# Performance work log

Measured on AMD Instinct MI355X. Metric: run time of the kernel, lower is better.

Reference implementation:

```python
import jax, jax.numpy as jnp
import numpy as np

CHANNELS = [4096, 4096, 4096, 4096]
SPARSITY = 0.9  # fraction of weight entries zeroed (sten.random_mask_sparsify frac)
BATCH = 4096


def _sparse_weight(key, out_f, in_f, frac):
    kw, km = jax.random.split(key)
    w = jax.random.normal(kw, (out_f, in_f), dtype=jnp.float32)
    keep = jax.random.uniform(km, (out_f, in_f)) >= frac  # keep ~(1-frac) entries
    return jnp.where(keep, w, 0.0)


def setup_inputs() -> dict:
    key = jax.random.key(0)
    ks = jax.random.split(key, 7)
    x = jax.random.normal(ks[0], (BATCH, CHANNELS[0]), dtype=jnp.float32)
    W1 = _sparse_weight(ks[1], CHANNELS[1], CHANNELS[0], SPARSITY)
    b1 = jax.random.uniform(ks[2], (CHANNELS[1],), dtype=jnp.float32)
    W2 = _sparse_weight(ks[3], CHANNELS[2], CHANNELS[1], SPARSITY)
    b2 = jax.random.uniform(ks[4], (CHANNELS[2],), dtype=jnp.float32)
    W3 = _sparse_weight(ks[5], CHANNELS[3], CHANNELS[2], SPARSITY)
    b3 = jax.random.uniform(ks[6], (CHANNELS[3],), dtype=jnp.float32)
    return {"x": x, "W1": W1, "b1": b1, "W2": W2, "b2": b2, "W3": W3, "b3": b3}


def reference(x, W1, b1, W2, b2, W3, b3):
    # Sequential: Linear -> ReLU -> Linear -> ReLU -> Linear
    # F.linear(x, W, b) == x @ W.T + b; weights already carry the sparsity mask.
    h = x @ W1.T + b1
    h = jax.nn.relu(h)
    h = h @ W2.T + b2
    h = jax.nn.relu(h)
    return h @ W3.T + b3
```

## Files before the change

kernel.cpp:

```cpp
#include <hip/hip_runtime.h>
#include <cstdint>


#define MATN 4096
#define NT (MATN / 64)

typedef _Float16 half8 __attribute__((ext_vector_type(8)));
typedef float f32x4 __attribute__((ext_vector_type(4)));

__device__ __forceinline__ void glds16(const void* g, void* l) {
    __builtin_amdgcn_global_load_lds(
        (const __attribute__((address_space(1))) char*)(uintptr_t)g,
        (__attribute__((address_space(3))) char*)(uintptr_t)l,
        16, 0, 0);
}

__device__ __forceinline__ void cvtblk_body(const float* __restrict__ in,
                                            _Float16* __restrict__ out, int n16) {
    for (int g = blockIdx.x * 256 + threadIdx.x; g < n16; g += gridDim.x * 256) {
        const int r16 = g & 15;
        const int kq  = (g >> 4) & 3;
        const int ks  = (g >> 6) & 1;
        const int T   = (g >> 7) & 63;
        const int R   = g >> 13;
        const size_t row = (size_t)R * 16 + r16;
        const int    col = T * 64 + ks * 32 + kq * 8;
        const float* p = in + row * MATN + col;
        float4 a = *(const float4*)p;
        float4 b = *(const float4*)(p + 4);
        half8 o;
        o[0] = (_Float16)a.x; o[1] = (_Float16)a.y;
        o[2] = (_Float16)a.z; o[3] = (_Float16)a.w;
        o[4] = (_Float16)b.x; o[5] = (_Float16)b.y;
        o[6] = (_Float16)b.z; o[7] = (_Float16)b.w;
        *(half8*)(out + (size_t)g * 8) = o;
    }
}

__global__ __launch_bounds__(256)
void cvt_blk(const float* __restrict__ in, _Float16* __restrict__ out, int n16) {
    cvtblk_body(in, out, n16);
}

__global__ __launch_bounds__(256)
void cvt_blk2(const float* __restrict__ i0, _Float16* __restrict__ o0,
              const float* __restrict__ i1, _Float16* __restrict__ o1, int n16) {
    cvtblk_body(blockIdx.y ? i1 : i0, blockIdx.y ? o1 : o0, n16);
}

__global__ __launch_bounds__(256)
void cvt_blk4(const float* __restrict__ i0, _Float16* __restrict__ o0,
              const float* __restrict__ i1, _Float16* __restrict__ o1,
              const float* __restrict__ i2, _Float16* __restrict__ o2,
              const float* __restrict__ i3, _Float16* __restrict__ o3, int n16) {
    const float* in;
    _Float16* out;
    switch (blockIdx.y) {
        case 0: in = i0; out = o0; break;
        case 1: in = i1; out = o1; break;
        case 2: in = i2; out = o2; break;
        default: in = i3; out = o3; break;
    }
    cvtblk_body(in, out, n16);
}

#define MFMA_(d, x, y) d = __builtin_amdgcn_mfma_f32_16x16x32_f16(x, y, d, 0, 0, 0)

template <bool RELU, bool OBLK, typename OutT>
__global__ __launch_bounds__(512, 2)
void gemm_blk(const _Float16* __restrict__ A, const _Float16* __restrict__ B,
              const float* __restrict__ bias, OutT* __restrict__ C) {
    __shared__ _Float16 lds[2][4][128 * 64];

    const int tid  = threadIdx.x;
    const int lane = tid & 63;
    const int w    = tid >> 6;
    const int wm   = w >> 2;
    const int wn   = w & 3;
    const int l16  = lane & 15;
    const int kq   = lane >> 4;

    const int bid   = blockIdx.y * 16 + blockIdx.x;
    const int sbid  = (bid & 7) * 32 + (bid >> 3);
    const int tileM = (sbid >> 4) * 256;
    const int tileN = (sbid & 15) * 256;

    char* const ldsb = (char*)lds;

    const int lb = lane * 16;
    const char* const aSrc =
        (const char*)A + ((size_t)((tileM >> 4) + w) * 131072) + lb;
    const char* const bSrc =
        (const char*)B + ((size_t)((tileN >> 4) + w) * 131072) + lb;
    const int wj = w * 2048;

#define SA(Tt, h, j)                                                           \
    do {                                                                       \
        if ((Tt) < NT)                                                         \
            glds16(aSrc + (size_t)(h)*1048576 + (size_t)(Tt)*2048 + (j)*1024,  \
                   ldsb + ((Tt)&1) * 65536 + (h)*49152 + wj + (j)*1024);       \
    } while (0)
#define SB(Tt, h, j)                                                           \
    do {                                                                       \
        if ((Tt) < NT)                                                         \
            glds16(bSrc + (size_t)(h)*1048576 + (size_t)(Tt)*2048 + (j)*1024,  \
                   ldsb + ((Tt)&1) * 65536 + 16384 + (h)*16384 + wj +          \
                       (j)*1024);                                              \
    } while (0)

    half8 aP[4], bP[4], bQ[4];
    f32x4 acc[8][4] = {};

    SA(0, 0, 0); SA(0, 1, 0);
    SB(0, 0, 0); SB(0, 1, 0);
    SA(0, 0, 1); SA(0, 1, 1);
    SB(0, 0, 1); SB(0, 1, 1);
    asm volatile("s_waitcnt vmcnt(4)" ::: "memory");
    __builtin_amdgcn_s_barrier();

    for (int T = 0; T < NT; ++T) {
        const char* bufb = ldsb + (T & 1) * 65536;
        const char* Ard  = bufb + wm * 49152 + lb;
        const char* Brd  = bufb + 16384 + (wn >> 1) * 16384 + (wn & 1) * 8192 + lb;

#pragma unroll
        for (int i = 0; i < 4; ++i) aP[i] = *(const half8*)(Ard + i * 2048);
#pragma unroll
        for (int n = 0; n < 4; ++n) bP[n] = *(const half8*)(Brd + n * 2048);
        SA(T + 1, 0, 0); SA(T + 1, 1, 0);
        __builtin_amdgcn_s_barrier();
        asm volatile("s_waitcnt lgkmcnt(0)" ::: "memory");
        __builtin_amdgcn_sched_barrier(0);
        __builtin_amdgcn_s_setprio(1);
#pragma unroll
        for (int i = 0; i < 4; ++i)
#pragma unroll
            for (int n = 0; n < 4; ++n) MFMA_(acc[i][n], aP[i], bP[n]);
        __builtin_amdgcn_s_setprio(0);
        __builtin_amdgcn_s_barrier();

#pragma unroll
        for (int i = 0; i < 4; ++i)
            aP[i] = *(const half8*)(Ard + 8192 + i * 2048);
        SB(T + 1, 0, 0); SB(T + 1, 1, 0);
        __builtin_amdgcn_s_barrier();
        asm volatile("s_waitcnt lgkmcnt(0)" ::: "memory");
        __builtin_amdgcn_sched_barrier(0);
        __builtin_amdgcn_s_setprio(1);
#pragma unroll
        for (int i = 0; i < 4; ++i)
#pragma unroll
            for (int n = 0; n < 4; ++n) MFMA_(acc[4 + i][n], aP[i], bP[n]);
        __builtin_amdgcn_s_setprio(0);
        if (T < NT - 1)
            asm volatile("s_waitcnt vmcnt(4)" ::: "memory");
        else
            asm volatile("s_waitcnt vmcnt(0)" ::: "memory");
        __builtin_amdgcn_s_barrier();

#pragma unroll
        for (int i = 0; i < 4; ++i)
            aP[i] = *(const half8*)(Ard + 9216 + i * 2048);
#pragma unroll
        for (int n = 0; n < 4; ++n)
            bQ[n] = *(const half8*)(Brd + 1024 + n * 2048);
        SA(T + 1, 0, 1); SA(T + 1, 1, 1);
        __builtin_amdgcn_s_barrier();
        asm volatile("s_waitcnt lgkmcnt(0)" ::: "memory");
        __builtin_amdgcn_sched_barrier(0);
        __builtin_amdgcn_s_setprio(1);
#pragma unroll
        for (int i = 0; i < 4; ++i)
#pragma unroll
            for (int n = 0; n < 4; ++n) MFMA_(acc[4 + i][n], aP[i], bQ[n]);
        __builtin_amdgcn_s_setprio(0);
        __builtin_amdgcn_s_barrier();

#pragma unroll
        for (int i = 0; i < 4; ++i)
            aP[i] = *(const half8*)(Ard + 1024 + i * 2048);
        SB(T + 1, 0, 1); SB(T + 1, 1, 1);
        __builtin_amdgcn_s_barrier();
        asm volatile("s_waitcnt lgkmcnt(0)" ::: "memory");
        __builtin_amdgcn_sched_barrier(0);
        __builtin_amdgcn_s_setprio(1);
#pragma unroll
        for (int i = 0; i < 4; ++i)
#pragma unroll
            for (int n = 0; n < 4; ++n) MFMA_(acc[i][n], aP[i], bQ[n]);
        __builtin_amdgcn_s_setprio(0);
        asm volatile("s_waitcnt vmcnt(4)" ::: "memory");
        __builtin_amdgcn_s_barrier();
    }
#undef SA
#undef SB

    if (OBLK) {
        char* const Cb = (char*)C;
        const int tN0 = tileN >> 6;
#pragma unroll
        for (int ni = 0; ni < 4; ++ni) {
            const int q  = ni * 16 + l16;
            const float bv = bias[tileN + wn * 64 + q];
            const size_t colOff = (size_t)(((tN0 + wn) * 2 + ((q >> 5) & 1))) * 1024 +
                                  ((q >> 3) & 3) * 256 + (q & 7) * 2;
#pragma unroll
            for (int mi = 0; mi < 8; ++mi) {
                const size_t Roff =
                    (size_t)((tileM >> 4) + wm * 8 + mi) * 131072;
#pragma unroll
                for (int r = 0; r < 4; ++r) {
                    float v = acc[mi][ni][r] + bv;
                    if (RELU) v = v > 0.f ? v : 0.f;
                    *(_Float16*)(Cb + Roff + colOff + (kq * 4 + r) * 16) =
                        (_Float16)v;
                }
            }
        }
    } else {
#pragma unroll
        for (int ni = 0; ni < 4; ++ni) {
            const int gn = tileN + wn * 64 + ni * 16 + l16;
            const float bv = bias[gn];
#pragma unroll
            for (int mi = 0; mi < 8; ++mi) {
                const int gm = tileM + wm * 128 + mi * 16 + kq * 4;
#pragma unroll
                for (int r = 0; r < 4; ++r) {
                    float v = acc[mi][ni][r] + bv;
                    if (RELU) v = v > 0.f ? v : 0.f;
                    C[(size_t)(gm + r) * MATN + gn] = (OutT)v;
                }
            }
        }
    }
}

extern "C" void kernel_launch(void* const* d_in, const int* in_sizes, int n_in,
                              void* d_out, int out_size, void* d_ws, size_t ws_size,
                              hipStream_t stream) {
    const float* x  = (const float*)d_in[0];
    const float* W1 = (const float*)d_in[1];
    const float* b1 = (const float*)d_in[2];
    const float* W2 = (const float*)d_in[3];
    const float* b2 = (const float*)d_in[4];
    const float* W3 = (const float*)d_in[5];
    const float* b3 = (const float*)d_in[6];
    float* out = (float*)d_out;

    const size_t MAT = (size_t)MATN * MATN;
    const size_t HB  = MAT * 2;
    const int n16 = (int)(MAT / 8);
    dim3 ggrid(MATN / 256, MATN / 256);

    if (ws_size >= HB * 5) {
        _Float16* xb = (_Float16*)d_ws;
        _Float16* w1 = (_Float16*)((char*)d_ws + HB);
        _Float16* w2 = (_Float16*)((char*)d_ws + HB * 2);
        _Float16* w3 = (_Float16*)((char*)d_ws + HB * 3);
        _Float16* h1 = (_Float16*)((char*)d_ws + HB * 4);
        _Float16* h2 = xb;

        cvt_blk4<<<dim3(8192, 4), 256, 0, stream>>>(x, xb, W1, w1, W2, w2,
                                                    W3, w3, n16);
        gemm_blk<true, true, _Float16><<<ggrid, 512, 0, stream>>>(xb, w1, b1, h1);
        gemm_blk<true, true, _Float16><<<ggrid, 512, 0, stream>>>(h1, w2, b2, h2);
        gemm_blk<false, false, float><<<ggrid, 512, 0, stream>>>(h2, w3, b3, out);
    } else {
        _Float16* xb = (_Float16*)d_ws;
        _Float16* wb = (_Float16*)((char*)d_ws + HB);
        _Float16* h1 = (_Float16*)((char*)d_ws + HB * 2);
        _Float16* h2 = xb;

        cvt_blk2<<<dim3(8192, 2), 256, 0, stream>>>(x, xb, W1, wb, n16);
        gemm_blk<true, true, _Float16><<<ggrid, 512, 0, stream>>>(xb, wb, b1, h1);
        cvt_blk<<<8192, 256, 0, stream>>>(W2, wb, n16);
        gemm_blk<true, true, _Float16><<<ggrid, 512, 0, stream>>>(h1, wb, b2, h2);
        cvt_blk<<<8192, 256, 0, stream>>>(W3, wb, n16);
        gemm_blk<false, false, float><<<ggrid, 512, 0, stream>>>(h2, wb, b3, out);
    }
}
```

Baseline: 577.9 us.

## Load A fragments directly into registers, stage only B in LDS

The GEMM now loads each wave's A operand straight from global memory into registers, since every wave owns distinct rows, and stages only the B tile in LDS. This halves LDS capacity and traffic and removes most per-phase barriers. The wave layout changes from 2x4 to 4x2, with each wave covering 64x128. The conversion kernel is reorganised so each wave handles one 512-element block unit, and the grid is shrunk to match. Trade-offs: more VGPR pressure from the extra prefetch registers, and A global-load latency now sits directly on the MFMA dependency chain.

```diff
diff --git a/kernel.cpp b/kernel.cpp
--- a/kernel.cpp
+++ b/kernel.cpp
@@ -16,16 +16,16 @@
 }
 
 __device__ __forceinline__ void cvtblk_body(const float* __restrict__ in,
-                                            _Float16* __restrict__ out, int n16) {
-    for (int g = blockIdx.x * 256 + threadIdx.x; g < n16; g += gridDim.x * 256) {
-        const int r16 = g & 15;
-        const int kq  = (g >> 4) & 3;
-        const int ks  = (g >> 6) & 1;
-        const int T   = (g >> 7) & 63;
-        const int R   = g >> 13;
-        const size_t row = (size_t)R * 16 + r16;
-        const int    col = T * 64 + ks * 32 + kq * 8;
-        const float* p = in + row * MATN + col;
+                                            _Float16* __restrict__ out,
+                                            int nunits) {
+    const int lane = threadIdx.x & 63;
+    const int r16 = lane & 15, kq = lane >> 4;
+    const int wv = (blockIdx.x * 256 + (int)threadIdx.x) >> 6;
+    const int nw = (gridDim.x * 256) >> 6;
+    for (int u = wv; u < nunits; u += nw) {
+        const int ks = u & 1, T = (u >> 1) & 63, R = u >> 7;
+        const float* p =
+            in + (size_t)(R * 16 + r16) * MATN + T * 64 + ks * 32 + kq * 8;
         float4 a = *(const float4*)p;
         float4 b = *(const float4*)(p + 4);
         half8 o;
@@ -33,26 +33,26 @@
         o[2] = (_Float16)a.z; o[3] = (_Float16)a.w;
         o[4] = (_Float16)b.x; o[5] = (_Float16)b.y;
         o[6] = (_Float16)b.z; o[7] = (_Float16)b.w;
-        *(half8*)(out + (size_t)g * 8) = o;
+        *(half8*)(out + (size_t)u * 512 + lane * 8) = o;
     }
 }
 
 __global__ __launch_bounds__(256)
-void cvt_blk(const float* __restrict__ in, _Float16* __restrict__ out, int n16) {
-    cvtblk_body(in, out, n16);
+void cvt_blk(const float* __restrict__ in, _Float16* __restrict__ out, int nu) {
+    cvtblk_body(in, out, nu);
 }
 
 __global__ __launch_bounds__(256)
 void cvt_blk2(const float* __restrict__ i0, _Float16* __restrict__ o0,
-              const float* __restrict__ i1, _Float16* __restrict__ o1, int n16) {
-    cvtblk_body(blockIdx.y ? i1 : i0, blockIdx.y ? o1 : o0, n16);
+              const float* __restrict__ i1, _Float16* __restrict__ o1, int nu) {
+    cvtblk_body(blockIdx.y ? i1 : i0, blockIdx.y ? o1 : o0, nu);
 }
 
 __global__ __launch_bounds__(256)
 void cvt_blk4(const float* __restrict__ i0, _Float16* __restrict__ o0,
               const float* __restrict__ i1, _Float16* __restrict__ o1,
               const float* __restrict__ i2, _Float16* __restrict__ o2,
-              const float* __restrict__ i3, _Float16* __restrict__ o3, int n16) {
+              const float* __restrict__ i3, _Float16* __restrict__ o3, int nu) {
     const float* in;
     _Float16* out;
     switch (blockIdx.y) {
@@ -61,22 +61,22 @@
         case 2: in = i2; out = o2; break;
         default: in = i3; out = o3; break;
     }
-    cvtblk_body(in, out, n16);
+    cvtblk_body(in, out, nu);
 }
 
 #define MFMA_(d, x, y) d = __builtin_amdgcn_mfma_f32_16x16x32_f16(x, y, d, 0, 0, 0)
 
 template <bool RELU, bool OBLK, typename OutT>
 __global__ __launch_bounds__(512, 2)
-void gemm_blk(const _Float16* __restrict__ A, const _Float16* __restrict__ B,
-              const float* __restrict__ bias, OutT* __restrict__ C) {
-    __shared__ _Float16 lds[2][4][128 * 64];
+void gemm_areg(const _Float16* __restrict__ A, const _Float16* __restrict__ B,
+               const float* __restrict__ bias, OutT* __restrict__ C) {
+    __shared__ _Float16 ldsB[2][16384];
 
     const int tid  = threadIdx.x;
     const int lane = tid & 63;
     const int w    = tid >> 6;
-    const int wm   = w >> 2;
-    const int wn   = w & 3;
+    const int wm   = w >> 1;
+    const int wn   = w & 1;
     const int l16  = lane & 15;
     const int kq   = lane >> 4;
 
@@ -85,132 +85,125 @@
     const int tileM = (sbid >> 4) * 256;
     const int tileN = (sbid & 15) * 256;
 
-    char* const ldsb = (char*)lds;
-
+    char* const ldsb = (char*)ldsB;
     const int lb = lane * 16;
-    const char* const aSrc =
-        (const char*)A + ((size_t)((tileM >> 4) + w) * 131072) + lb;
+
     const char* const bSrc =
-        (const char*)B + ((size_t)((tileN >> 4) + w) * 131072) + lb;
-    const int wj = w * 2048;
-
-#define SA(Tt, h, j)                                                           \
+        (const char*)B + (size_t)((tileN >> 4) + w) * 131072 + lb;
+#define SB(Tt, g, j)                                                           \
     do {                                                                       \
         if ((Tt) < NT)                                                         \
-            glds16(aSrc + (size_t)(h)*1048576 + (size_t)(Tt)*2048 + (j)*1024,  \
-                   ldsb + ((Tt)&1) * 65536 + (h)*49152 + wj + (j)*1024);       \
+            glds16(bSrc + (size_t)(g)*1048576 + (size_t)(Tt)*2048 + (j)*1024,  \
+                   ldsb + ((Tt)&1) * 32768 + ((g)*8 + w) * 2048 + (j)*1024);   \
     } while (0)
-#define SB(Tt, h, j)                                                           \
+
+    const char* const aSrc =
+        (const char*)A + (size_t)((tileM >> 4) + wm * 4) * 131072 + lb;
+#define LA(dst, Tt, ks_)                                                       \
     do {                                                                       \
-        if ((Tt) < NT)                                                         \
-            glds16(bSrc + (size_t)(h)*1048576 + (size_t)(Tt)*2048 + (j)*1024,  \
-                   ldsb + ((Tt)&1) * 65536 + 16384 + (h)*16384 + wj +          \
-                       (j)*1024);                                              \
+        if ((Tt) < NT) {                                                       \
+            _Pragma("unroll") for (int i_ = 0; i_ < 4; ++i_) dst[i_] =         \
+                *(const half8*)(aSrc + (size_t)i_ * 131072 +                   \
+                                (size_t)(Tt)*2048 + (ks_)*1024);               \
+        }                                                                      \
     } while (0)
 
-    half8 aP[4], bP[4], bQ[4];
-    f32x4 acc[8][4] = {};
-
-    SA(0, 0, 0); SA(0, 1, 0);
-    SB(0, 0, 0); SB(0, 1, 0);
-    SA(0, 0, 1); SA(0, 1, 1);
-    SB(0, 0, 1); SB(0, 1, 1);
-    asm volatile("s_waitcnt vmcnt(4)" ::: "memory");
+    half8 aA[4], aB[4], b[8];
+    f32x4 acc[4][8] = {};
+
+    SB(0, 0, 0); SB(0, 1, 0); SB(0, 0, 1); SB(0, 1, 1);
+    LA(aA, 0, 0);
+    LA(aB, 0, 1);
+    asm volatile("s_waitcnt vmcnt(8)" ::: "memory");
     __builtin_amdgcn_s_barrier();
 
+#pragma unroll 2
     for (int T = 0; T < NT; ++T) {
-        const char* bufb = ldsb + (T & 1) * 65536;
-        const char* Ard  = bufb + wm * 49152 + lb;
-        const char* Brd  = bufb + 16384 + (wn >> 1) * 16384 + (wn & 1) * 8192 + lb;
-
-#pragma unroll
-        for (int i = 0; i < 4; ++i) aP[i] = *(const half8*)(Ard + i * 2048);
-#pragma unroll
-        for (int n = 0; n < 4; ++n) bP[n] = *(const half8*)(Brd + n * 2048);
-        SA(T + 1, 0, 0); SA(T + 1, 1, 0);
-        __builtin_amdgcn_s_barrier();
-        asm volatile("s_waitcnt lgkmcnt(0)" ::: "memory");
-        __builtin_amdgcn_sched_barrier(0);
-        __builtin_amdgcn_s_setprio(1);
-#pragma unroll
-        for (int i = 0; i < 4; ++i)
-#pragma unroll
-            for (int n = 0; n < 4; ++n) MFMA_(acc[i][n], aP[i], bP[n]);
-        __builtin_amdgcn_s_setprio(0);
-        __builtin_amdgcn_s_barrier();
-
-#pragma unroll
-        for (int i = 0; i < 4; ++i)
-            aP[i] = *(const half8*)(Ard + 8192 + i * 2048);
+        const char* Brd = ldsb + (T & 1) * 32768 + wn * 16384 + lb;
+
+#pragma unroll
+        for (int n = 0; n < 4; ++n) b[n] = *(const half8*)(Brd + n * 2048);
         SB(T + 1, 0, 0); SB(T + 1, 1, 0);
-        __builtin_amdgcn_s_barrier();
-        asm volatile("s_waitcnt lgkmcnt(0)" ::: "memory");
-        __builtin_amdgcn_sched_barrier(0);
-        __builtin_amdgcn_s_setprio(1);
-#pragma unroll
-        for (int i = 0; i < 4; ++i)
-#pragma unroll
-            for (int n = 0; n < 4; ++n) MFMA_(acc[4 + i][n], aP[i], bP[n]);
-        __builtin_amdgcn_s_setprio(0);
+        asm volatile("s_waitcnt vmcnt(6)" ::: "memory");
+        asm volatile("s_waitcnt lgkmcnt(0)" ::: "memory");
+        __builtin_amdgcn_sched_barrier(0);
+        __builtin_amdgcn_s_setprio(1);
+#pragma unroll
+        for (int i = 0; i < 4; ++i)
+#pragma unroll
+            for (int n = 0; n < 4; ++n) MFMA_(acc[i][n], aA[i], b[n]);
+        __builtin_amdgcn_s_setprio(0);
+
+#pragma unroll
+        for (int n = 0; n < 4; ++n)
+            b[4 + n] = *(const half8*)(Brd + (4 + n) * 2048);
+        asm volatile("s_waitcnt lgkmcnt(0)" ::: "memory");
+        __builtin_amdgcn_sched_barrier(0);
+        __builtin_amdgcn_s_setprio(1);
+#pragma unroll
+        for (int i = 0; i < 4; ++i)
+#pragma unroll
+            for (int n = 0; n < 4; ++n) MFMA_(acc[i][4 + n], aA[i], b[4 + n]);
+        __builtin_amdgcn_s_setprio(0);
+        LA(aA, T + 1, 0);
+
+        if (T < NT - 1)
+            asm volatile("s_waitcnt vmcnt(6)" ::: "memory");
+        else
+            asm volatile("s_waitcnt vmcnt(0)" ::: "memory");
+
+#pragma unroll
+        for (int n = 0; n < 4; ++n)
+            b[4 + n] = *(const half8*)(Brd + (4 + n) * 2048 + 1024);
+        SB(T + 1, 0, 1); SB(T + 1, 1, 1);
+        asm volatile("s_waitcnt lgkmcnt(0)" ::: "memory");
+        __builtin_amdgcn_sched_barrier(0);
+        __builtin_amdgcn_s_setprio(1);
+#pragma unroll
+        for (int i = 0; i < 4; ++i)
+#pragma unroll
+            for (int n = 0; n < 4; ++n) MFMA_(acc[i][4 + n], aB[i], b[4 + n]);
+        __builtin_amdgcn_s_setprio(0);
+
+#pragma unroll
+        for (int n = 0; n < 4; ++n)
+            b[n] = *(const half8*)(Brd + n * 2048 + 1024);
+        asm volatile("s_waitcnt lgkmcnt(0)" ::: "memory");
+        __builtin_amdgcn_sched_barrier(0);
+        __builtin_amdgcn_s_setprio(1);
+#pragma unroll
+        for (int i = 0; i < 4; ++i)
+#pragma unroll
+            for (int n = 0; n < 4; ++n) MFMA_(acc[i][n], aB[i], b[n]);
+        __builtin_amdgcn_s_setprio(0);
+        LA(aB, T + 1, 1);
+
         if (T < NT - 1)
             asm volatile("s_waitcnt vmcnt(4)" ::: "memory");
         else
             asm volatile("s_waitcnt vmcnt(0)" ::: "memory");
         __builtin_amdgcn_s_barrier();
-
-#pragma unroll
-        for (int i = 0; i < 4; ++i)
-            aP[i] = *(const half8*)(Ard + 9216 + i * 2048);
-#pragma unroll
-        for (int n = 0; n < 4; ++n)
-            bQ[n] = *(const half8*)(Brd + 1024 + n * 2048);
-        SA(T + 1, 0, 1); SA(T + 1, 1, 1);
-        __builtin_amdgcn_s_barrier();
-        asm volatile("s_waitcnt lgkmcnt(0)" ::: "memory");
-        __builtin_amdgcn_sched_barrier(0);
-        __builtin_amdgcn_s_setprio(1);
-#pragma unroll
-        for (int i = 0; i < 4; ++i)
-#pragma unroll
-            for (int n = 0; n < 4; ++n) MFMA_(acc[4 + i][n], aP[i], bQ[n]);
-        __builtin_amdgcn_s_setprio(0);
-        __builtin_amdgcn_s_barrier();
-
-#pragma unroll
-        for (int i = 0; i < 4; ++i)
-            aP[i] = *(const half8*)(Ard + 1024 + i * 2048);
-        SB(T + 1, 0, 1); SB(T + 1, 1, 1);
-        __builtin_amdgcn_s_barrier();
-        asm volatile("s_waitcnt lgkmcnt(0)" ::: "memory");
-        __builtin_amdgcn_sched_barrier(0);
-        __builtin_amdgcn_s_setprio(1);
-#pragma unroll
-        for (int i = 0; i < 4; ++i)
-#pragma unroll
-            for (int n = 0; n < 4; ++n) MFMA_(acc[i][n], aP[i], bQ[n]);
-        __builtin_amdgcn_s_setprio(0);
-        asm volatile("s_waitcnt vmcnt(4)" ::: "memory");
-        __builtin_amdgcn_s_barrier();
-    }
-#undef SA
+    }
 #undef SB
+#undef LA
 
     if (OBLK) {
         char* const Cb = (char*)C;
-        const int tN0 = tileN >> 6;
-#pragma unroll
-        for (int ni = 0; ni < 4; ++ni) {
-            const int q  = ni * 16 + l16;
-            const float bv = bias[tileN + wn * 64 + q];
-            const size_t colOff = (size_t)(((tN0 + wn) * 2 + ((q >> 5) & 1))) * 1024 +
-                                  ((q >> 3) & 3) * 256 + (q & 7) * 2;
-#pragma unroll
-            for (int mi = 0; mi < 8; ++mi) {
+#pragma unroll
+        for (int n = 0; n < 8; ++n) {
+            const int cw = n * 16 + l16;
+            const int gn = tileN + wn * 128 + cw;
+            const float bv = bias[gn];
+            const size_t colOff = (size_t)((tileN >> 6) + wn * 2 + (n >> 2)) * 2048 +
+                                  ((n >> 1) & 1) * 1024 + (n & 1) * 512 +
+                                  (l16 >> 3) * 256 + (l16 & 7) * 2;
+#pragma unroll
+            for (int i = 0; i < 4; ++i) {
                 const size_t Roff =
-                    (size_t)((tileM >> 4) + wm * 8 + mi) * 131072;
+                    (size_t)((tileM >> 4) + wm * 4 + i) * 131072;
 #pragma unroll
                 for (int r = 0; r < 4; ++r) {
-                    float v = acc[mi][ni][r] + bv;
+                    float v = acc[i][n][r] + bv;
                     if (RELU) v = v > 0.f ? v : 0.f;
                     *(_Float16*)(Cb + Roff + colOff + (kq * 4 + r) * 16) =
                         (_Float16)v;
@@ -219,15 +212,15 @@
         }
     } else {
 #pragma unroll
-        for (int ni = 0; ni < 4; ++ni) {
-            const int gn = tileN + wn * 64 + ni * 16 + l16;
+        for (int n = 0; n < 8; ++n) {
+            const int gn = tileN + wn * 128 + n * 16 + l16;
             const float bv = bias[gn];
 #pragma unroll
-            for (int mi = 0; mi < 8; ++mi) {
-                const int gm = tileM + wm * 128 + mi * 16 + kq * 4;
+            for (int i = 0; i < 4; ++i) {
+                const int gm = tileM + wm * 64 + i * 16 + kq * 4;
 #pragma unroll
                 for (int r = 0; r < 4; ++r) {
-                    float v = acc[mi][ni][r] + bv;
+                    float v = acc[i][n][r] + bv;
                     if (RELU) v = v > 0.f ? v : 0.f;
                     C[(size_t)(gm + r) * MATN + gn] = (OutT)v;
                 }
@@ -250,7 +243,7 @@
 
     const size_t MAT = (size_t)MATN * MATN;
     const size_t HB  = MAT * 2;
-    const int n16 = (int)(MAT / 8);
+    const int nu = (int)(MAT / 512);
     dim3 ggrid(MATN / 256, MATN / 256);
 
     if (ws_size >= HB * 5) {
@@ -261,22 +254,22 @@
         _Float16* h1 = (_Float16*)((char*)d_ws + HB * 4);
         _Float16* h2 = xb;
 
-        cvt_blk4<<<dim3(8192, 4), 256, 0, stream>>>(x, xb, W1, w1, W2, w2,
-                                                    W3, w3, n16);
-        gemm_blk<true, true, _Float16><<<ggrid, 512, 0, stream>>>(xb, w1, b1, h1);
-        gemm_blk<true, true, _Float16><<<ggrid, 512, 0, stream>>>(h1, w2, b2, h2);
-        gemm_blk<false, false, float><<<ggrid, 512, 0, stream>>>(h2, w3, b3, out);
+        cvt_blk4<<<dim3(2048, 4), 256, 0, stream>>>(x, xb, W1, w1, W2, w2,
+                                                    W3, w3, nu);
+        gemm_areg<true, true, _Float16><<<ggrid, 512, 0, stream>>>(xb, w1, b1, h1);
+        gemm_areg<true, true, _Float16><<<ggrid, 512, 0, stream>>>(h1, w2, b2, h2);
+        gemm_areg<false, false, float><<<ggrid, 512, 0, stream>>>(h2, w3, b3, out);
     } else {
         _Float16* xb = (_Float16*)d_ws;
         _Float16* wb = (_Float16*)((char*)d_ws + HB);
         _Float16* h1 = (_Float16*)((char*)d_ws + HB * 2);
         _Float16* h2 = xb;
 
-        cvt_blk2<<<dim3(8192, 2), 256, 0, stream>>>(x, xb, W1, wb, n16);
-        gemm_blk<true, true, _Float16><<<ggrid, 512, 0, stream>>>(xb, wb, b1, h1);
-        cvt_blk<<<8192, 256, 0, stream>>>(W2, wb, n16);
-        gemm_blk<true, true, _Float16><<<ggrid, 512, 0, stream>>>(h1, wb, b2, h2);
-        cvt_blk<<<8192, 256, 0, stream>>>(W3, wb, n16);
-        gemm_blk<false, false, float><<<ggrid, 512, 0, stream>>>(h2, wb, b3, out);
-    }
-}
+        cvt_blk2<<<dim3(2048, 2), 256, 0, stream>>>(x, xb, W1, wb, nu);
+        gemm_areg<true, true, _Float16><<<ggrid, 512, 0, stream>>>(xb, wb, b1, h1);
+        cvt_blk<<<2048, 256, 0, stream>>>(W2, wb, nu);
+        gemm_areg<true, true, _Float16><<<ggrid, 512, 0, stream>>>(h1, wb, b2, h2);
+        cvt_blk<<<2048, 256, 0, stream>>>(W3, wb, nu);
+        gemm_areg<false, false, float><<<ggrid, 512, 0, stream>>>(h2, wb, b3, out);
+    }
+}
```

After: 640.6 us. +10.8%, slower.
